# Kernel optimization log

Hardware: AMD Instinct MI355X
Metric: run time of the kernel (lower is better)

The kernel has to match this reference:

```python
import jax, jax.numpy as jnp
import numpy as np

D_MODEL = 1024
N_HEADS = 16
HEAD_DIM = D_MODEL // N_HEADS


def setup_inputs() -> dict:
    key = jax.random.key(0)
    ks = jax.random.split(key, 5)
    T, B = 2048, 2
    x = jax.random.normal(ks[0], (T, B, D_MODEL), dtype=jnp.float32)
    s = 1.0 / np.sqrt(D_MODEL)
    Wq = jax.random.normal(ks[1], (D_MODEL, D_MODEL), dtype=jnp.float32) * s
    Wk = jax.random.normal(ks[2], (D_MODEL, D_MODEL), dtype=jnp.float32) * s
    Wv = jax.random.normal(ks[3], (D_MODEL, D_MODEL), dtype=jnp.float32) * s
    Wo = jax.random.normal(ks[4], (D_MODEL, D_MODEL), dtype=jnp.float32) * s
    return {"x": x, "Wq": Wq, "Wk": Wk, "Wv": Wv, "Wo": Wo}


def reference(x, Wq, Wk, Wv, Wo):
    T, B, C = x.shape
    H, D = N_HEADS, HEAD_DIM

    def split_heads(t):
        # (T,B,C) -> (B,H,T,D), matching view+permute(1,2,0,3)
        return t.reshape(T, B, H, D).transpose(1, 2, 0, 3)

    q = split_heads(x @ Wq.T)
    k = split_heads(x @ Wk.T)
    v = split_heads(x @ Wv.T)

    scale = 1.0 / jnp.sqrt(jnp.asarray(D, dtype=x.dtype))
    scores = jnp.einsum('bhqd,bhkd->bhqk', q, k) * scale  # (B,H,T,T)
    causal = jnp.tril(jnp.ones((T, T), dtype=bool))
    scores = jnp.where(causal, scores, jnp.asarray(-jnp.inf, dtype=scores.dtype))
    probs = jax.nn.softmax(scores, axis=-1)
    ctx = jnp.einsum('bhqk,bhkd->bhqd', probs, v)  # (B,H,T,D)
    ctx = ctx.transpose(2, 0, 1, 3).reshape(T, B, C)
    return ctx @ Wo.T
```

## Files before the change

### kernel.cpp

```cpp
#include <hip/hip_runtime.h>
#include <hip/hip_bf16.h>

#define TT 2048
#define BB 2
#define CC 1024
#define HH 16
#define DD 64
#define MM (TT * BB)

typedef short bf16x8 __attribute__((ext_vector_type(8)));
typedef float f32x4  __attribute__((ext_vector_type(4)));

__device__ inline ushort f2b(float f) {
    union { float f; unsigned u; } v; v.f = f;
    unsigned r = v.u + 0x7FFFu + ((v.u >> 16) & 1u);
    return (ushort)(r >> 16);
}

__device__ inline unsigned pack_bf16(float a, float b) {
    __hip_bfloat162 h = __float22bfloat162_rn(make_float2(a, b));
    union { __hip_bfloat162 h; unsigned u; } c; c.h = h;
    return c.u;
}

__device__ inline void gload_lds16(const ushort* g, ushort* l) {
    __builtin_amdgcn_global_load_lds(
        (const __attribute__((address_space(1))) void*)g,
        (__attribute__((address_space(3))) void*)l, 16, 0, 0);
}

#define XQUADS (MM * CC / 4)
#define WQUADS (CC * CC / 4)
__global__ __launch_bounds__(256) void conv_all(const float* __restrict__ x,
                                                const float* __restrict__ Wq,
                                                const float* __restrict__ Wk,
                                                const float* __restrict__ Wv,
                                                const float* __restrict__ Wo,
                                                ushort* __restrict__ dst) {
    int idx = blockIdx.x * 256 + threadIdx.x;
    const float* src;
    int off;
    if (idx < XQUADS) {
        src = x; off = idx;
    } else {
        int wi = (idx - XQUADS) >> 18;
        off = (idx - XQUADS) & (WQUADS - 1);
        src = (wi == 0) ? Wq : (wi == 1) ? Wk : (wi == 2) ? Wv : Wo;
    }
    float4 v = ((const float4*)src)[off];
    ushort4 o = {f2b(v.x), f2b(v.y), f2b(v.z), f2b(v.w)};
    ((ushort4*)dst)[idx] = o;
}

__global__ __launch_bounds__(256) void gemm_qkv(const ushort* __restrict__ A,
                                                const ushort* __restrict__ B0,
                                                const ushort* __restrict__ B1,
                                                const ushort* __restrict__ B2,
                                                ushort* __restrict__ Oq,
                                                ushort* __restrict__ Ok,
                                                ushort* __restrict__ Ov) {
    __shared__ __align__(16) ushort As[128 * 32];
    __shared__ __align__(16) ushort Bs[128 * 32];

    const int tid = threadIdx.x;
    const int wave = tid >> 6, lane = tid & 63;
    const int quad = lane >> 4, l16 = lane & 15;
    const int wm = wave >> 1, wn = wave & 1;

    const int bm = blockIdx.x * 128;
    const int by = blockIdx.y;
    const int wsel = by >> 3;
    const ushort* Bp = (wsel == 0) ? B0 : (wsel == 1) ? B1 : B2;
    const int bn = (by & 7) * 128;

    const int srow = lane >> 2;
    const int scol = (lane & 3) * 8;

    f32x4 acc[4][4];
#pragma unroll
    for (int i = 0; i < 4; i++)
#pragma unroll
        for (int j = 0; j < 4; j++) acc[i][j] = (f32x4){0.f, 0.f, 0.f, 0.f};

    for (int k0 = 0; k0 < CC; k0 += 32) {
#pragma unroll
        for (int i = 0; i < 2; i++) {
            const int rbase = wave * 32 + i * 16;
            gload_lds16(A + (size_t)(bm + rbase + srow) * CC + k0 + scol,
                        As + rbase * 32);
            gload_lds16(Bp + (size_t)(bn + rbase + srow) * CC + k0 + scol,
                        Bs + rbase * 32);
        }
        __syncthreads();

        bf16x8 af[4], bf[4];
#pragma unroll
        for (int mi = 0; mi < 4; mi++)
            af[mi] = *(const bf16x8*)(As + (wm * 64 + mi * 16 + l16) * 32 + quad * 8);
#pragma unroll
        for (int ni = 0; ni < 4; ni++)
            bf[ni] = *(const bf16x8*)(Bs + (wn * 64 + ni * 16 + l16) * 32 + quad * 8);
#pragma unroll
        for (int mi = 0; mi < 4; mi++)
#pragma unroll
            for (int ni = 0; ni < 4; ni++)
                acc[mi][ni] = __builtin_amdgcn_mfma_f32_16x16x32_bf16(
                    af[mi], bf[ni], acc[mi][ni], 0, 0, 0);
        __syncthreads();
    }

#pragma unroll
    for (int mi = 0; mi < 4; mi++) {
#pragma unroll
        for (int r = 0; r < 4; r++) {
            const int m = bm + wm * 64 + mi * 16 + quad * 4 + r;
#pragma unroll
            for (int ni = 0; ni < 4; ni++) {
                const int colg = bn + wn * 64 + ni * 16 + l16;
                float v = acc[mi][ni][r];
                if (wsel == 0) v *= 0.18033688f;
                const int t = m >> 1, b = m & 1;
                const int h = colg >> 6, d = colg & 63;
                ushort* dst = (wsel == 0) ? Oq : (wsel == 1) ? Ok : Ov;
                dst[(((size_t)(b * HH + h)) * TT + t) * DD + d] = f2b(v);
            }
        }
    }
}

__global__ __launch_bounds__(256) void gemm_out(const ushort* __restrict__ A,
                                                const ushort* __restrict__ Bm,
                                                float* __restrict__ Of) {
    __shared__ __align__(16) ushort As[128 * 32];
    __shared__ __align__(16) ushort Bs[64 * 32];

    const int tid = threadIdx.x;
    const int wave = tid >> 6, lane = tid & 63;
    const int quad = lane >> 4, l16 = lane & 15;

    const int bm = blockIdx.x * 128;
    const int bn = blockIdx.y * 64;

    const int srow = lane >> 2;
    const int scol = (lane & 3) * 8;

    f32x4 acc[2][4];
#pragma unroll
    for (int i = 0; i < 2; i++)
#pragma unroll
        for (int j = 0; j < 4; j++) acc[i][j] = (f32x4){0.f, 0.f, 0.f, 0.f};

    for (int k0 = 0; k0 < CC; k0 += 32) {
#pragma unroll
        for (int i = 0; i < 2; i++) {
            const int rbase = wave * 32 + i * 16;
            gload_lds16(A + (size_t)(bm + rbase + srow) * CC + k0 + scol,
                        As + rbase * 32);
        }
        gload_lds16(Bm + (size_t)(bn + wave * 16 + srow) * CC + k0 + scol,
                    Bs + wave * 16 * 32);
        __syncthreads();

        bf16x8 af[2], bf[4];
#pragma unroll
        for (int mi = 0; mi < 2; mi++)
            af[mi] = *(const bf16x8*)(As + (wave * 32 + mi * 16 + l16) * 32 + quad * 8);
#pragma unroll
        for (int ni = 0; ni < 4; ni++)
            bf[ni] = *(const bf16x8*)(Bs + (ni * 16 + l16) * 32 + quad * 8);
#pragma unroll
        for (int mi = 0; mi < 2; mi++)
#pragma unroll
            for (int ni = 0; ni < 4; ni++)
                acc[mi][ni] = __builtin_amdgcn_mfma_f32_16x16x32_bf16(
                    af[mi], bf[ni], acc[mi][ni], 0, 0, 0);
        __syncthreads();
    }

#pragma unroll
    for (int mi = 0; mi < 2; mi++)
#pragma unroll
        for (int r = 0; r < 4; r++) {
            const int m = bm + wave * 32 + mi * 16 + quad * 4 + r;
#pragma unroll
            for (int ni = 0; ni < 4; ni++)
                Of[(size_t)m * CC + bn + ni * 16 + l16] = acc[mi][ni][r];
        }
}

__global__ __launch_bounds__(256) void vtrans(const ushort* __restrict__ Vb,
                                              ushort* __restrict__ Vt) {
    __shared__ __align__(16) ushort Ls[64 * 80];
    const int bh = blockIdx.y;
    const int t0 = blockIdx.x * 64;
    const int e = threadIdx.x;
    const size_t bsrc = (size_t)bh * TT * DD;
    const size_t bdst = (size_t)bh * DD * TT;

#pragma unroll
    for (int p = 0; p < 2; p++) {
        int r = p * 32 + (e >> 3);
        int oct = e & 7;
        *(uint4*)(Ls + r * 80 + oct * 8) =
            *(const uint4*)(Vb + bsrc + (size_t)(t0 + r) * DD + oct * 8);
    }
    __syncthreads();
#pragma unroll
    for (int p = 0; p < 2; p++) {
        int d = p * 32 + (e >> 3);
        int toct = e & 7;
        ushort tmp[8];
#pragma unroll
        for (int u = 0; u < 8; u++) {
            int jp = toct * 8 + u;
            int js = (jp & 3) * 16 + (jp >> 2);
            tmp[u] = Ls[js * 80 + d];
        }
        *(uint4*)(Vt + bdst + (size_t)d * TT + t0 + toct * 8) = *(uint4*)tmp;
    }
}

template <int AM, bool BD>
__device__ __forceinline__ void attn_step2(const bf16x8* qaA, const bf16x8* qaB,
                                           f32x4* OA, f32x4* OB,
                                           float* lA, float* lB,
                                           const ushort* Ks, const ushort* Vs,
                                           ushort* PA, ushort* PB,
                                           int j0, int q0A, int q0B,
                                           int quad, int l16) {
    f32x4 SA[4], SB[4];
#pragma unroll
    for (int nb = 0; nb < 4; nb++) {
        SB[nb] = (f32x4){0.f, 0.f, 0.f, 0.f};
        if (AM < 2) SA[nb] = (f32x4){0.f, 0.f, 0.f, 0.f};
    }
#pragma unroll
    for (int c = 0; c < 2; c++)
#pragma unroll
        for (int nb = 0; nb < 4; nb++) {
            bf16x8 k = *(const bf16x8*)(Ks + (nb * 16 + l16) * 72 + c * 32 + quad * 8);
            SB[nb] = __builtin_amdgcn_mfma_f32_16x16x32_bf16(qaB[c], k, SB[nb], 0, 0, 0);
            if (AM < 2)
                SA[nb] = __builtin_amdgcn_mfma_f32_16x16x32_bf16(qaA[c], k, SA[nb], 0, 0, 0);
        }

#pragma unroll
    for (int r = 0; r < 4; r++) {
        {
            const int qg = q0B + quad * 4 + r;
            float p[4];
#pragma unroll
            for (int nb = 0; nb < 4; nb++) {
                float s = SB[nb][r];
                if (BD) { if (j0 + nb * 16 + l16 > qg) s = -1e30f; }
                p[nb] = __builtin_amdgcn_exp2f(fminf(s, 60.f));
            }
            lB[r] += (p[0] + p[1]) + (p[2] + p[3]);
            uint2 w; w.x = pack_bf16(p[0], p[1]); w.y = pack_bf16(p[2], p[3]);
            *(uint2*)(PB + (quad * 4 + r) * 72 + l16 * 4) = w;
        }
        if (AM < 2) {
            const int qg = q0A + quad * 4 + r;
            float p[4];
#pragma unroll
            for (int nb = 0; nb < 4; nb++) {
                float s = SA[nb][r];
                if (AM == 1) { if (j0 + nb * 16 + l16 > qg) s = -1e30f; }
                p[nb] = __builtin_amdgcn_exp2f(fminf(s, 60.f));
            }
            lA[r] += (p[0] + p[1]) + (p[2] + p[3]);
            uint2 w; w.x = pack_bf16(p[0], p[1]); w.y = pack_bf16(p[2], p[3]);
            *(uint2*)(PA + (quad * 4 + r) * 72 + l16 * 4) = w;
        }
    }

#pragma unroll
    for (int c = 0; c < 2; c++) {
        bf16x8 paB = *(const bf16x8*)(PB + l16 * 72 + c * 32 + quad * 8);
        bf16x8 paA;
        if (AM < 2) paA = *(const bf16x8*)(PA + l16 * 72 + c * 32 + quad * 8);
#pragma unroll
        for (int db = 0; db < 4; db++) {
            bf16x8 v = *(const bf16x8*)(Vs + (db * 16 + l16) * 72 + c * 32 + quad * 8);
            OB[db] = __builtin_amdgcn_mfma_f32_16x16x32_bf16(paB, v, OB[db], 0, 0, 0);
            if (AM < 2)
                OA[db] = __builtin_amdgcn_mfma_f32_16x16x32_bf16(paA, v, OA[db], 0, 0, 0);
        }
    }
}

__global__ __launch_bounds__(256, 2) void attn_mfma(const ushort* __restrict__ Qb,
                                                    const ushort* __restrict__ Kb,
                                                    const ushort* __restrict__ Vt,
                                                    ushort* __restrict__ ctx) {
    __shared__ __align__(16) ushort Ks[64 * 72];
    __shared__ __align__(16) ushort Vs[64 * 72];
    __shared__ __align__(16) ushort PsA[4 * 16 * 72];
    __shared__ __align__(16) ushort PsB[4 * 16 * 72];

    const int tid  = threadIdx.x;
    const int wave = tid >> 6;
    const int lane = tid & 63;
    const int quad = lane >> 4;
    const int l16  = lane & 15;

    const int p  = blockIdx.x;
    const int bh = blockIdx.y;
    const int qtA = p, qtB = (TT / 64 - 1) - p;
    const int q0A = qtA * 64 + wave * 16;
    const int q0B = qtB * 64 + wave * 16;

    const size_t baseQK = (size_t)bh * TT * DD;
    const size_t baseVt = (size_t)bh * DD * TT;

    bf16x8 qaA[2], qaB[2];
    {
        const ushort* qp = Qb + baseQK + (size_t)(q0A + l16) * DD + quad * 8;
        qaA[0] = *(const bf16x8*)(qp);
        qaA[1] = *(const bf16x8*)(qp + 32);
        const ushort* qp2 = Qb + baseQK + (size_t)(q0B + l16) * DD + quad * 8;
        qaB[0] = *(const bf16x8*)(qp2);
        qaB[1] = *(const bf16x8*)(qp2 + 32);
    }

    f32x4 OA[4], OB[4];
#pragma unroll
    for (int i = 0; i < 4; i++) {
        OA[i] = (f32x4){0.f, 0.f, 0.f, 0.f};
        OB[i] = (f32x4){0.f, 0.f, 0.f, 0.f};
    }
    float lA[4] = {0.f, 0.f, 0.f, 0.f};
    float lB[4] = {0.f, 0.f, 0.f, 0.f};

    ushort* PA = PsA + wave * 16 * 72;
    ushort* PB = PsB + wave * 16 * 72;

    const int row0 = tid >> 3;
    const int oct  = tid & 7;

    uint4 kr0, kr1, vr0, vr1;
    kr0 = *(const uint4*)(Kb + baseQK + (size_t)row0 * DD + oct * 8);
    kr1 = *(const uint4*)(Kb + baseQK + (size_t)(row0 + 32) * DD + oct * 8);
    vr0 = *(const uint4*)(Vt + baseVt + (size_t)row0 * TT + oct * 8);
    vr1 = *(const uint4*)(Vt + baseVt + (size_t)(row0 + 32) * TT + oct * 8);

    for (int kt = 0; kt <= qtB; kt++) {
        const int j0 = kt * 64;

        *(uint4*)(Ks + row0 * 72 + oct * 8) = kr0;
        *(uint4*)(Ks + (row0 + 32) * 72 + oct * 8) = kr1;
        *(uint4*)(Vs + row0 * 72 + oct * 8) = vr0;
        *(uint4*)(Vs + (row0 + 32) * 72 + oct * 8) = vr1;
        __syncthreads();

        if (kt < qtB) {
            const int jn = j0 + 64;
            kr0 = *(const uint4*)(Kb + baseQK + (size_t)(jn + row0) * DD + oct * 8);
            kr1 = *(const uint4*)(Kb + baseQK + (size_t)(jn + row0 + 32) * DD + oct * 8);
            vr0 = *(const uint4*)(Vt + baseVt + (size_t)row0 * TT + jn + oct * 8);
            vr1 = *(const uint4*)(Vt + baseVt + (size_t)(row0 + 32) * TT + jn + oct * 8);
        }

        if (kt < qtA)
            attn_step2<0, false>(qaA, qaB, OA, OB, lA, lB, Ks, Vs, PA, PB,
                                 j0, q0A, q0B, quad, l16);
        else if (kt == qtA)
            attn_step2<1, false>(qaA, qaB, OA, OB, lA, lB, Ks, Vs, PA, PB,
                                 j0, q0A, q0B, quad, l16);
        else if (kt < qtB)
            attn_step2<2, false>(qaA, qaB, OA, OB, lA, lB, Ks, Vs, PA, PB,
                                 j0, q0A, q0B, quad, l16);
        else
            attn_step2<2, true>(qaA, qaB, OA, OB, lA, lB, Ks, Vs, PA, PB,
                                j0, q0A, q0B, quad, l16);
        __syncthreads();
    }

    const int b = bh >> 4, h = bh & 15;
#pragma unroll
    for (int r = 0; r < 4; r++) {
        float la = lA[r], lb = lB[r];
        la += __shfl_xor(la, 1); la += __shfl_xor(la, 2);
        la += __shfl_xor(la, 4); la += __shfl_xor(la, 8);
        lb += __shfl_xor(lb, 1); lb += __shfl_xor(lb, 2);
        lb += __shfl_xor(lb, 4); lb += __shfl_xor(lb, 8);
        const float invA = 1.f / la;
        const float invB = 1.f / lb;
        const int tA = q0A + quad * 4 + r;
        const int tB = q0B + quad * 4 + r;
#pragma unroll
        for (int db = 0; db < 4; db++) {
            ctx[((size_t)tA * BB + b) * CC + h * DD + db * 16 + l16] =
                f2b(OA[db][r] * invA);
            ctx[((size_t)tB * BB + b) * CC + h * DD + db * 16 + l16] =
                f2b(OB[db][r] * invB);
        }
    }
}

extern "C" void kernel_launch(void* const* d_in, const int* in_sizes, int n_in,
                              void* d_out, int out_size, void* d_ws, size_t ws_size,
                              hipStream_t stream) {
    const float* x  = (const float*)d_in[0];
    const float* Wq = (const float*)d_in[1];
    const float* Wk = (const float*)d_in[2];
    const float* Wv = (const float*)d_in[3];
    const float* Wo = (const float*)d_in[4];
    float* out = (float*)d_out;

    ushort* xb  = (ushort*)d_ws;
    ushort* Wb  = xb + (size_t)MM * CC;
    ushort* Wqb = Wb;
    ushort* Wkb = Wb + (size_t)CC * CC;
    ushort* Wvb = Wb + 2 * (size_t)CC * CC;
    ushort* Wob = Wb + 3 * (size_t)CC * CC;
    ushort* Qb  = Wb + 4 * (size_t)CC * CC;
    ushort* Kb  = Qb + (size_t)MM * CC;
    ushort* Vb  = Kb + (size_t)MM * CC;
    ushort* Vt  = Vb + (size_t)MM * CC;
    ushort* Ctxb = Vt + (size_t)MM * CC;

    conv_all<<<dim3((XQUADS + 4 * WQUADS) / 256), 256, 0, stream>>>(
        x, Wq, Wk, Wv, Wo, xb);

    gemm_qkv<<<dim3(MM / 128, 24), 256, 0, stream>>>(
        xb, Wqb, Wkb, Wvb, Qb, Kb, Vb);

    vtrans<<<dim3(TT / 64, BB * HH), 256, 0, stream>>>(Vb, Vt);

    attn_mfma<<<dim3(TT / 128, BB * HH), 256, 0, stream>>>(Qb, Kb, Vt, Ctxb);

    gemm_out<<<dim3(MM / 128, CC / 64), 256, 0, stream>>>(Ctxb, Wob, out);
}
```

Measured before the change: 182.2 us.

## Load K/V MFMA fragments directly from global memory, drop LDS staging and barriers

Removes shared-memory staging of the K and V tiles. Each wave now loads its MFMA operand fragments straight from global memory (relying on L1/L2 for reuse across the four waves), and both __syncthreads per key tile are gone. It also drops the fminf clamp before exp2. In exchange, each wave issues its own redundant global loads with no software prefetch, so latency is exposed at the start of each step, and global traffic through the cache rises roughly fourfold.

```diff
diff --git a/kernel.cpp b/kernel.cpp
--- a/kernel.cpp
+++ b/kernel.cpp
@@ -224,10 +224,20 @@
 __device__ __forceinline__ void attn_step2(const bf16x8* qaA, const bf16x8* qaB,
                                            f32x4* OA, f32x4* OB,
                                            float* lA, float* lB,
-                                           const ushort* Ks, const ushort* Vs,
+                                           const ushort* __restrict__ Kg,
+                                           const ushort* __restrict__ Vg,
                                            ushort* PA, ushort* PB,
                                            int j0, int q0A, int q0B,
                                            int quad, int l16) {
+    bf16x8 kf[8], vf[8];
+#pragma unroll
+    for (int c = 0; c < 2; c++)
+#pragma unroll
+        for (int nb = 0; nb < 4; nb++) {
+            kf[c * 4 + nb] = *(const bf16x8*)(Kg + (size_t)(nb * 16 + l16) * DD + c * 32 + quad * 8);
+            vf[c * 4 + nb] = *(const bf16x8*)(Vg + (size_t)(nb * 16 + l16) * TT + c * 32 + quad * 8);
+        }
+
     f32x4 SA[4], SB[4];
 #pragma unroll
     for (int nb = 0; nb < 4; nb++) {
@@ -238,10 +248,9 @@
     for (int c = 0; c < 2; c++)
 #pragma unroll
         for (int nb = 0; nb < 4; nb++) {
-            bf16x8 k = *(const bf16x8*)(Ks + (nb * 16 + l16) * 72 + c * 32 + quad * 8);
-            SB[nb] = __builtin_amdgcn_mfma_f32_16x16x32_bf16(qaB[c], k, SB[nb], 0, 0, 0);
+            SB[nb] = __builtin_amdgcn_mfma_f32_16x16x32_bf16(qaB[c], kf[c * 4 + nb], SB[nb], 0, 0, 0);
             if (AM < 2)
-                SA[nb] = __builtin_amdgcn_mfma_f32_16x16x32_bf16(qaA[c], k, SA[nb], 0, 0, 0);
+                SA[nb] = __builtin_amdgcn_mfma_f32_16x16x32_bf16(qaA[c], kf[c * 4 + nb], SA[nb], 0, 0, 0);
         }
 
 #pragma unroll
@@ -253,7 +262,7 @@
             for (int nb = 0; nb < 4; nb++) {
                 float s = SB[nb][r];
                 if (BD) { if (j0 + nb * 16 + l16 > qg) s = -1e30f; }
-                p[nb] = __builtin_amdgcn_exp2f(fminf(s, 60.f));
+                p[nb] = __builtin_amdgcn_exp2f(s);
             }
             lB[r] += (p[0] + p[1]) + (p[2] + p[3]);
             uint2 w; w.x = pack_bf16(p[0], p[1]); w.y = pack_bf16(p[2], p[3]);
@@ -266,7 +275,7 @@
             for (int nb = 0; nb < 4; nb++) {
                 float s = SA[nb][r];
                 if (AM == 1) { if (j0 + nb * 16 + l16 > qg) s = -1e30f; }
-                p[nb] = __builtin_amdgcn_exp2f(fminf(s, 60.f));
+                p[nb] = __builtin_amdgcn_exp2f(s);
             }
             lA[r] += (p[0] + p[1]) + (p[2] + p[3]);
             uint2 w; w.x = pack_bf16(p[0], p[1]); w.y = pack_bf16(p[2], p[3]);
@@ -281,10 +290,9 @@
         if (AM < 2) paA = *(const bf16x8*)(PA + l16 * 72 + c * 32 + quad * 8);
 #pragma unroll
         for (int db = 0; db < 4; db++) {
-            bf16x8 v = *(const bf16x8*)(Vs + (db * 16 + l16) * 72 + c * 32 + quad * 8);
-            OB[db] = __builtin_amdgcn_mfma_f32_16x16x32_bf16(paB, v, OB[db], 0, 0, 0);
+            OB[db] = __builtin_amdgcn_mfma_f32_16x16x32_bf16(paB, vf[c * 4 + db], OB[db], 0, 0, 0);
             if (AM < 2)
-                OA[db] = __builtin_amdgcn_mfma_f32_16x16x32_bf16(paA, v, OA[db], 0, 0, 0);
+                OA[db] = __builtin_amdgcn_mfma_f32_16x16x32_bf16(paA, vf[c * 4 + db], OA[db], 0, 0, 0);
         }
     }
 }
@@ -293,8 +301,6 @@
                                                     const ushort* __restrict__ Kb,
                                                     const ushort* __restrict__ Vt,
                                                     ushort* __restrict__ ctx) {
-    __shared__ __align__(16) ushort Ks[64 * 72];
-    __shared__ __align__(16) ushort Vs[64 * 72];
     __shared__ __align__(16) ushort PsA[4 * 16 * 72];
     __shared__ __align__(16) ushort PsB[4 * 16 * 72];
 
@@ -335,45 +341,27 @@
     ushort* PA = PsA + wave * 16 * 72;
     ushort* PB = PsB + wave * 16 * 72;
 
-    const int row0 = tid >> 3;
-    const int oct  = tid & 7;
-
-    uint4 kr0, kr1, vr0, vr1;
-    kr0 = *(const uint4*)(Kb + baseQK + (size_t)row0 * DD + oct * 8);
-    kr1 = *(const uint4*)(Kb + baseQK + (size_t)(row0 + 32) * DD + oct * 8);
-    vr0 = *(const uint4*)(Vt + baseVt + (size_t)row0 * TT + oct * 8);
-    vr1 = *(const uint4*)(Vt + baseVt + (size_t)(row0 + 32) * TT + oct * 8);
+    const ushort* Kg = Kb + baseQK;
+    const ushort* Vg = Vt + baseVt;
 
     for (int kt = 0; kt <= qtB; kt++) {
         const int j0 = kt * 64;
 
-        *(uint4*)(Ks + row0 * 72 + oct * 8) = kr0;
-        *(uint4*)(Ks + (row0 + 32) * 72 + oct * 8) = kr1;
-        *(uint4*)(Vs + row0 * 72 + oct * 8) = vr0;
-        *(uint4*)(Vs + (row0 + 32) * 72 + oct * 8) = vr1;
-        __syncthreads();
-
-        if (kt < qtB) {
-            const int jn = j0 + 64;
-            kr0 = *(const uint4*)(Kb + baseQK + (size_t)(jn + row0) * DD + oct * 8);
-            kr1 = *(const uint4*)(Kb + baseQK + (size_t)(jn + row0 + 32) * DD + oct * 8);
-            vr0 = *(const uint4*)(Vt + baseVt + (size_t)row0 * TT + jn + oct * 8);
-            vr1 = *(const uint4*)(Vt + baseVt + (size_t)(row0 + 32) * TT + jn + oct * 8);
-        }
-
         if (kt < qtA)
-            attn_step2<0, false>(qaA, qaB, OA, OB, lA, lB, Ks, Vs, PA, PB,
+            attn_step2<0, false>(qaA, qaB, OA, OB, lA, lB, Kg, Vg, PA, PB,
                                  j0, q0A, q0B, quad, l16);
         else if (kt == qtA)
-            attn_step2<1, false>(qaA, qaB, OA, OB, lA, lB, Ks, Vs, PA, PB,
+            attn_step2<1, false>(qaA, qaB, OA, OB, lA, lB, Kg, Vg, PA, PB,
                                  j0, q0A, q0B, quad, l16);
         else if (kt < qtB)
-            attn_step2<2, false>(qaA, qaB, OA, OB, lA, lB, Ks, Vs, PA, PB,
+            attn_step2<2, false>(qaA, qaB, OA, OB, lA, lB, Kg, Vg, PA, PB,
                                  j0, q0A, q0B, quad, l16);
         else
-            attn_step2<2, true>(qaA, qaB, OA, OB, lA, lB, Ks, Vs, PA, PB,
+            attn_step2<2, true>(qaA, qaB, OA, OB, lA, lB, Kg, Vg, PA, PB,
                                 j0, q0A, q0B, quad, l16);
-        __syncthreads();
+
+        Kg += 64 * DD;
+        Vg += 64;
     }
 
     const int b = bh >> 4, h = bh & 15;
```

New measurement: 253.7 us. 1.39x slower.
